# Kernel optimization log

Measured on AMD Instinct MI355X. Metric: run time of the kernel, lower is better.

Reference implementation:

```python
import jax, jax.numpy as jnp
import numpy as np

N = 131072
EPOCHS = 1000
INLIER_THRESH = 10.0  # hardcoded in original torch.le(dis, 10)


def rigid_fit_2d(A, B, w):
    """Weighted least-squares 2D Euclidean (rotation+translation) fit.
    A, B: [k, 2] corresponding points; w: [k] weights.
    Returns (rot, u, v) minimizing sum w * ||R(rot) a + t - b||^2.
    """
    ws = jnp.maximum(w.sum(), 1e-8)
    cA = (w[:, None] * A).sum(0) / ws  # [2]
    cB = (w[:, None] * B).sum(0) / ws
    A0 = A - cA
    B0 = B - cB
    sxx = (w * (A0[:, 0] * B0[:, 0] + A0[:, 1] * B0[:, 1])).sum()
    sxy = (w * (A0[:, 0] * B0[:, 1] - A0[:, 1] * B0[:, 0])).sum()
    rot = jnp.arctan2(sxy, sxx)
    c, s = jnp.cos(rot), jnp.sin(rot)
    u = cB[0] - (c * cA[0] - s * cA[1])
    v = cB[1] - (s * cA[0] + c * cA[1])
    return rot, u, v


def euclidean_matrix(rot, u, v):
    c, s = jnp.cos(rot), jnp.sin(rot)
    zero = jnp.zeros_like(u)
    one = jnp.ones_like(u)
    return jnp.stack([
        jnp.stack([c, -s, u]),
        jnp.stack([s, c, v]),
        jnp.stack([zero, zero, one]),
    ])  # [3,3]


def setup_inputs() -> dict:
    key = jax.random.key(0)
    k1, k2, k3 = jax.random.split(key, 3)
    pstA = jax.random.normal(k1, (1, N, 2), dtype=jnp.float32)
    pstB = jax.random.normal(k2, (1, N, 2), dtype=jnp.float32)
    subset_idx = jax.random.randint(k3, (EPOCHS, 5), 0, N, dtype=jnp.int32)
    return {"pstA": pstA, "pstB": pstB, "subset_idx": subset_idx}


def reference(pstA, pstB, subset_idx):
    A = pstA[0]  # [N,2]  (original code indexes batch 0)
    B = pstB[0]

    # --- batched hypothesis generation: fit 2D rigid transform per epoch ---
    subA = A[subset_idx]  # [E,5,2]
    subB = B[subset_idx]
    w5 = jnp.ones((5,), dtype=A.dtype)
    rot, u, v = jax.vmap(lambda a, b: rigid_fit_2d(a, b, w5))(subA, subB)  # each [E]

    # --- batched scoring: geometric distance of all N points per hypothesis ---
    c, s = jnp.cos(rot)[:, None], jnp.sin(rot)[:, None]  # [E,1]
    xA, yA = A[:, 0][None, :], A[:, 1][None, :]          # [1,N]
    xB, yB = B[:, 0][None, :], B[:, 1][None, :]
    errx = xB - (c * xA - s * yA + u[:, None])  # [E,N]
    erry = yB - (s * xA + c * yA + v[:, None])
    dis = jnp.sqrt(errx * errx + erry * erry)
    inliers = dis <= INLIER_THRESH  # [E,N]
    counts = inliers.sum(axis=1)

    # --- pick best hypothesis (replaces sequential best-so-far + early exit) ---
    best = jnp.argmax(counts)
    E_best = euclidean_matrix(rot[best], u[best], v[best])  # [3,3]

    # --- final refit on the inliers of the best hypothesis (mask as weights) ---
    w = inliers[best].astype(A.dtype)  # [N]
    rot_f, u_f, v_f = rigid_fit_2d(A, B, w)
    E_final = euclidean_matrix(rot_f, u_f, v_f)

    return jnp.stack([E_final, E_best])  # [2,3,3]
```

## Files before the change

### kernel.cpp

```cpp
#include <hip/hip_runtime.h>
#include <math.h>

#define N_PTS   131072
#define EPOCHS  1000
#define EPAD    1024
#define THRESH2 100.0f

#define SC_CHUNKS  512
#define SC_PTS     (N_PTS / SC_CHUNKS)
#define SC_THREADS 1024

#define RF_BLOCKS  256
#define RF_THREADS 256

#define OFF_H        0
#define OFF_PARTIAL  16384
#define OFF_PARTIAL2 1064960
#define OFF_BEST     1097728
#define OFF_RPART    1097744

__global__ void hypo_kernel(const float* __restrict__ A, const float* __restrict__ B,
                            const int* __restrict__ idx, float4* __restrict__ H) {
    int e = blockIdx.x * blockDim.x + threadIdx.x;
    if (e >= EPOCHS) return;

    float ax[5], ay[5], bx[5], by[5];
    float cAx = 0.f, cAy = 0.f, cBx = 0.f, cBy = 0.f;
#pragma unroll
    for (int j = 0; j < 5; ++j) {
        int p = idx[e * 5 + j];
        ax[j] = A[2 * p];     ay[j] = A[2 * p + 1];
        bx[j] = B[2 * p];     by[j] = B[2 * p + 1];
        cAx += ax[j]; cAy += ay[j];
        cBx += bx[j]; cBy += by[j];
    }
    cAx *= 0.2f; cAy *= 0.2f; cBx *= 0.2f; cBy *= 0.2f;

    float sxx = 0.f, sxy = 0.f;
#pragma unroll
    for (int j = 0; j < 5; ++j) {
        float a0x = ax[j] - cAx, a0y = ay[j] - cAy;
        float b0x = bx[j] - cBx, b0y = by[j] - cBy;
        sxx += a0x * b0x + a0y * b0y;
        sxy += a0x * b0y - a0y * b0x;
    }
    float rot = atan2f(sxy, sxx);
    float s, c;
    sincosf(rot, &s, &c);
    float u = cBx - (c * cAx - s * cAy);
    float v = cBy - (s * cAx + c * cAy);
    H[e] = make_float4(c, s, u, v);
}

#define EVAL(AX, AY, BX, BY)                                            \
    {                                                                   \
        float ex = fmaf(-c, (AX), fmaf(s, (AY), (BX) - u));             \
        float ey = fmaf(-s, (AX), fmaf(-c, (AY), (BY) - v));            \
        float d2 = fmaf(ex, ex, ey * ey);                               \
        cnt += (d2 <= THRESH2) ? 1 : 0;                                 \
    }

__global__ __launch_bounds__(SC_THREADS) void score_kernel(
        const float* __restrict__ A, const float* __restrict__ B,
        const float4* __restrict__ H, unsigned short* __restrict__ partial) {
    int tid = threadIdx.x;
    int chunk = blockIdx.x;
    float4 h = H[tid];
    float c = h.x, s = h.y, u = h.z, v = h.w;
    int cnt = 0;

    const float4* pA = (const float4*)A + chunk * (SC_PTS / 2);
    const float4* pB = (const float4*)B + chunk * (SC_PTS / 2);
    for (int t = 0; t < SC_PTS / 2; t += 4) {
        float4 a0 = pA[t + 0], a1 = pA[t + 1], a2 = pA[t + 2], a3 = pA[t + 3];
        float4 b0 = pB[t + 0], b1 = pB[t + 1], b2 = pB[t + 2], b3 = pB[t + 3];
        EVAL(a0.x, a0.y, b0.x, b0.y); EVAL(a0.z, a0.w, b0.z, b0.w);
        EVAL(a1.x, a1.y, b1.x, b1.y); EVAL(a1.z, a1.w, b1.z, b1.w);
        EVAL(a2.x, a2.y, b2.x, b2.y); EVAL(a2.z, a2.w, b2.z, b2.w);
        EVAL(a3.x, a3.y, b3.x, b3.y); EVAL(a3.z, a3.w, b3.z, b3.w);
    }
    partial[chunk * EPAD + tid] = (unsigned short)cnt;
}

__global__ void reduce_counts_kernel(const unsigned short* __restrict__ partial,
                                     int* __restrict__ partial2) {
    int gid = blockIdx.x * blockDim.x + threadIdx.x;
    int e = gid & (EPAD - 1);
    int g = gid >> 10;
    int s = 0;
    int base = g * 64;
#pragma unroll 8
    for (int k = 0; k < 64; ++k) s += partial[(base + k) * EPAD + e];
    partial2[g * EPAD + e] = s;
}

__global__ void argmax_kernel(const int* __restrict__ partial2, const float4* __restrict__ H,
                              float* __restrict__ out, float4* __restrict__ best) {
    __shared__ int scnt[256];
    __shared__ int sidx[256];
    int tid = threadIdx.x;
    int bc = -2, bi = 0;
    for (int e = tid; e < EPAD; e += 256) {
        int cv = -1;
        if (e < EPOCHS) {
            cv = 0;
#pragma unroll
            for (int g = 0; g < 8; ++g) cv += partial2[g * EPAD + e];
        }
        if (cv > bc) { bc = cv; bi = e; }
    }
    scnt[tid] = bc; sidx[tid] = bi;
    __syncthreads();
    for (int s2 = 128; s2 > 0; s2 >>= 1) {
        if (tid < s2) {
            int c2 = scnt[tid + s2], i2 = sidx[tid + s2];
            if (c2 > scnt[tid] || (c2 == scnt[tid] && i2 < sidx[tid])) {
                scnt[tid] = c2; sidx[tid] = i2;
            }
        }
        __syncthreads();
    }
    if (tid == 0) {
        float4 h = H[sidx[0]];
        *best = h;
        out[9]  = h.x;  out[10] = -h.y; out[11] = h.z;
        out[12] = h.y;  out[13] = h.x;  out[14] = h.w;
        out[15] = 0.f;  out[16] = 0.f;  out[17] = 1.f;
    }
}

__global__ __launch_bounds__(RF_THREADS) void refit_kernel(
        const float* __restrict__ A, const float* __restrict__ B,
        const float4* __restrict__ bestp, float* __restrict__ rpart) {
    float4 h = *bestp;
    float c = h.x, s = h.y, u = h.z, v = h.w;
    float m[9];
#pragma unroll
    for (int j = 0; j < 9; ++j) m[j] = 0.f;

    int gid = blockIdx.x * RF_THREADS + threadIdx.x;
    float4 a2 = ((const float4*)A)[gid];
    float4 b2 = ((const float4*)B)[gid];
#pragma unroll
    for (int k = 0; k < 2; ++k) {
        float ax = k ? a2.z : a2.x, ay = k ? a2.w : a2.y;
        float bx = k ? b2.z : b2.x, by = k ? b2.w : b2.y;
        float ex = fmaf(-c, ax, fmaf(s, ay, bx - u));
        float ey = fmaf(-s, ax, fmaf(-c, ay, by - v));
        float d2 = fmaf(ex, ex, ey * ey);
        if (d2 <= THRESH2) {
            m[0] += 1.f;
            m[1] += ax; m[2] += ay; m[3] += bx; m[4] += by;
            m[5] += ax * bx; m[6] += ax * by;
            m[7] += ay * bx; m[8] += ay * by;
        }
    }
#pragma unroll
    for (int off = 32; off > 0; off >>= 1)
#pragma unroll
        for (int j = 0; j < 9; ++j) m[j] += __shfl_down(m[j], off);

    __shared__ float sred[RF_THREADS / 64][9];
    int wave = threadIdx.x >> 6, lane = threadIdx.x & 63;
    if (lane == 0)
#pragma unroll
        for (int j = 0; j < 9; ++j) sred[wave][j] = m[j];
    __syncthreads();
    if (threadIdx.x == 0) {
#pragma unroll
        for (int j = 0; j < 9; ++j) {
            float t = sred[0][j] + sred[1][j] + sred[2][j] + sred[3][j];
            rpart[blockIdx.x * 16 + j] = t;
        }
    }
}

__global__ void finalize_kernel(const float* __restrict__ rpart, float* __restrict__ out) {
    int lane = threadIdx.x;
    float m[9];
#pragma unroll
    for (int j = 0; j < 9; ++j) m[j] = 0.f;
#pragma unroll
    for (int k = 0; k < 4; ++k)
#pragma unroll
        for (int j = 0; j < 9; ++j) m[j] += rpart[(lane + 64 * k) * 16 + j];
#pragma unroll
    for (int off = 32; off > 0; off >>= 1)
#pragma unroll
        for (int j = 0; j < 9; ++j) m[j] += __shfl_down(m[j], off);

    if (lane == 0) {
        float ws = fmaxf(m[0], 1e-8f);
        float cAx = m[1] / ws, cAy = m[2] / ws;
        float cBx = m[3] / ws, cBy = m[4] / ws;
        float sxx = (m[5] - ws * cAx * cBx) + (m[8] - ws * cAy * cBy);
        float sxy = (m[6] - ws * cAx * cBy) - (m[7] - ws * cAy * cBx);
        float rot = atan2f(sxy, sxx);
        float s, c;
        sincosf(rot, &s, &c);
        float u = cBx - (c * cAx - s * cAy);
        float v = cBy - (s * cAx + c * cAy);
        out[0] = c;   out[1] = -s;  out[2] = u;
        out[3] = s;   out[4] = c;   out[5] = v;
        out[6] = 0.f; out[7] = 0.f; out[8] = 1.f;
    }
}

extern "C" void kernel_launch(void* const* d_in, const int* in_sizes, int n_in,
                              void* d_out, int out_size, void* d_ws, size_t ws_size,
                              hipStream_t stream) {
    const float* A  = (const float*)d_in[0];
    const float* B  = (const float*)d_in[1];
    const int* sidx = (const int*)d_in[2];
    float* out = (float*)d_out;

    char* ws = (char*)d_ws;
    float4*         H        = (float4*)(ws + OFF_H);
    unsigned short* partial  = (unsigned short*)(ws + OFF_PARTIAL);
    int*            partial2 = (int*)(ws + OFF_PARTIAL2);
    float4*         best     = (float4*)(ws + OFF_BEST);
    float*          rpart    = (float*)(ws + OFF_RPART);

    hypo_kernel<<<4, 256, 0, stream>>>(A, B, sidx, H);
    score_kernel<<<SC_CHUNKS, SC_THREADS, 0, stream>>>(A, B, H, partial);
    reduce_counts_kernel<<<32, 256, 0, stream>>>(partial, partial2);
    argmax_kernel<<<1, 256, 0, stream>>>(partial2, H, out, best);
    refit_kernel<<<RF_BLOCKS, RF_THREADS, 0, stream>>>(A, B, best, rpart);
    finalize_kernel<<<1, 64, 0, stream>>>(rpart, out);
}
```

Measured before the change: 119.3 us.

## Stage points in LDS and assign four hypotheses per thread in scoring

The scoring kernel now loads a 128-point tile of A/B into shared memory as packed float4 and has each of 256 threads evaluate four hypotheses per point. Each point fetch is therefore reused across four hypotheses, cutting per-evaluation load instructions compared with every thread streaming global memory. Partial counts are stored as bytes, and the reduction now sums 128 rows per group to match the doubled block count. The costs are higher register pressure and a reliance on per-block counts staying at or below 255.

```diff
diff --git a/kernel.cpp b/kernel.cpp
--- a/kernel.cpp
+++ b/kernel.cpp
@@ -6,9 +6,9 @@
 #define EPAD    1024
 #define THRESH2 100.0f
 
-#define SC_CHUNKS  512
-#define SC_PTS     (N_PTS / SC_CHUNKS)
-#define SC_THREADS 1024
+#define SC_BLOCKS  1024
+#define SC_NT      256
+#define SC_PTS     (N_PTS / SC_BLOCKS)
 
 #define RF_BLOCKS  256
 #define RF_THREADS 256
@@ -52,45 +52,54 @@
     H[e] = make_float4(c, s, u, v);
 }
 
-#define EVAL(AX, AY, BX, BY)                                            \
-    {                                                                   \
-        float ex = fmaf(-c, (AX), fmaf(s, (AY), (BX) - u));             \
-        float ey = fmaf(-s, (AX), fmaf(-c, (AY), (BY) - v));            \
-        float d2 = fmaf(ex, ex, ey * ey);                               \
-        cnt += (d2 <= THRESH2) ? 1 : 0;                                 \
-    }
-
-__global__ __launch_bounds__(SC_THREADS) void score_kernel(
+#define EVAL(h, cnt)                                                        \
+    {                                                                       \
+        float ex = fmaf(-(h).x, p.x, fmaf((h).y, p.y, p.z - (h).z));        \
+        float ey = fmaf(-(h).y, p.x, fmaf(-(h).x, p.y, p.w - (h).w));       \
+        float d2 = fmaf(ex, ex, ey * ey);                                   \
+        cnt += (d2 <= THRESH2) ? 1 : 0;                                     \
+    }
+
+__global__ __launch_bounds__(SC_NT, 8) void score_kernel(
         const float* __restrict__ A, const float* __restrict__ B,
-        const float4* __restrict__ H, unsigned short* __restrict__ partial) {
+        const float4* __restrict__ H, unsigned char* __restrict__ partial) {
+    __shared__ float4 pts[SC_PTS];
     int tid = threadIdx.x;
-    int chunk = blockIdx.x;
-    float4 h = H[tid];
-    float c = h.x, s = h.y, u = h.z, v = h.w;
-    int cnt = 0;
-
-    const float4* pA = (const float4*)A + chunk * (SC_PTS / 2);
-    const float4* pB = (const float4*)B + chunk * (SC_PTS / 2);
-    for (int t = 0; t < SC_PTS / 2; t += 4) {
-        float4 a0 = pA[t + 0], a1 = pA[t + 1], a2 = pA[t + 2], a3 = pA[t + 3];
-        float4 b0 = pB[t + 0], b1 = pB[t + 1], b2 = pB[t + 2], b3 = pB[t + 3];
-        EVAL(a0.x, a0.y, b0.x, b0.y); EVAL(a0.z, a0.w, b0.z, b0.w);
-        EVAL(a1.x, a1.y, b1.x, b1.y); EVAL(a1.z, a1.w, b1.z, b1.w);
-        EVAL(a2.x, a2.y, b2.x, b2.y); EVAL(a2.z, a2.w, b2.z, b2.w);
-        EVAL(a3.x, a3.y, b3.x, b3.y); EVAL(a3.z, a3.w, b3.z, b3.w);
-    }
-    partial[chunk * EPAD + tid] = (unsigned short)cnt;
-}
-
-__global__ void reduce_counts_kernel(const unsigned short* __restrict__ partial,
+    int bid = blockIdx.x;
+
+    if (tid < SC_PTS) {
+        float2 a = ((const float2*)A)[bid * SC_PTS + tid];
+        float2 b = ((const float2*)B)[bid * SC_PTS + tid];
+        pts[tid] = make_float4(a.x, a.y, b.x, b.y);
+    }
+    float4 h0 = H[tid];
+    float4 h1 = H[tid + 256];
+    float4 h2 = H[tid + 512];
+    float4 h3 = H[tid + 768];
+    __syncthreads();
+
+    int c0 = 0, c1 = 0, c2 = 0, c3 = 0;
+#pragma unroll 4
+    for (int k = 0; k < SC_PTS; ++k) {
+        float4 p = pts[k];
+        EVAL(h0, c0); EVAL(h1, c1); EVAL(h2, c2); EVAL(h3, c3);
+    }
+    unsigned char* row = partial + bid * EPAD;
+    row[tid]       = (unsigned char)c0;
+    row[tid + 256] = (unsigned char)c1;
+    row[tid + 512] = (unsigned char)c2;
+    row[tid + 768] = (unsigned char)c3;
+}
+
+__global__ void reduce_counts_kernel(const unsigned char* __restrict__ partial,
                                      int* __restrict__ partial2) {
     int gid = blockIdx.x * blockDim.x + threadIdx.x;
     int e = gid & (EPAD - 1);
     int g = gid >> 10;
     int s = 0;
-    int base = g * 64;
+    int base = g * 128;
 #pragma unroll 8
-    for (int k = 0; k < 64; ++k) s += partial[(base + k) * EPAD + e];
+    for (int k = 0; k < 128; ++k) s += partial[(base + k) * EPAD + e];
     partial2[g * EPAD + e] = s;
 }
 
@@ -215,14 +224,14 @@
     float* out = (float*)d_out;
 
     char* ws = (char*)d_ws;
-    float4*         H        = (float4*)(ws + OFF_H);
-    unsigned short* partial  = (unsigned short*)(ws + OFF_PARTIAL);
-    int*            partial2 = (int*)(ws + OFF_PARTIAL2);
-    float4*         best     = (float4*)(ws + OFF_BEST);
-    float*          rpart    = (float*)(ws + OFF_RPART);
+    float4*        H        = (float4*)(ws + OFF_H);
+    unsigned char* partial  = (unsigned char*)(ws + OFF_PARTIAL);
+    int*           partial2 = (int*)(ws + OFF_PARTIAL2);
+    float4*        best     = (float4*)(ws + OFF_BEST);
+    float*         rpart    = (float*)(ws + OFF_RPART);
 
     hypo_kernel<<<4, 256, 0, stream>>>(A, B, sidx, H);
-    score_kernel<<<SC_CHUNKS, SC_THREADS, 0, stream>>>(A, B, H, partial);
+    score_kernel<<<SC_BLOCKS, SC_NT, 0, stream>>>(A, B, H, partial);
     reduce_counts_kernel<<<32, 256, 0, stream>>>(partial, partial2);
     argmax_kernel<<<1, 256, 0, stream>>>(partial2, H, out, best);
     refit_kernel<<<RF_BLOCKS, RF_THREADS, 0, stream>>>(A, B, best, rpart);
```

Result: slower. 155.0 us (+30.0%).
